# Optimization experiments

Hardware: AMD Instinct MI355X
Metric: run time of the kernel (lower is better)

## Reference

```python
import jax, jax.numpy as jnp
import numpy as np


def setup_inputs() -> dict:
    key = jax.random.key(0)
    k1, k2 = jax.random.split(key)
    B, L, J, N = 8, 32, 128, 512
    ypred = jax.random.normal(k1, (B, L, J, N), dtype=jnp.float32)
    xyz = jax.random.normal(k2, (B, L, N, 3), dtype=jnp.float32)
    return {"ypred": ypred, "xyz": xyz}


def _pairwise_dist(x):
    # x: [BL, N, 3] -> Euclidean distance [BL, N, N] via the mm trick,
    # with the diagonal forced to exactly 0 (matching torch.cdist(x, x)).
    sq = jnp.sum(x * x, axis=-1)                       # [BL, N]
    d2 = sq[:, :, None] + sq[:, None, :] - 2.0 * jnp.einsum('bnd,bmd->bnm', x, x)
    d2 = jnp.maximum(d2, 0.0)
    dist = jnp.sqrt(d2)
    n = x.shape[1]
    eye = jnp.eye(n, dtype=bool)
    return jnp.where(eye[None, :, :], 0.0, dist)


def reference(ypred, xyz):
    B, L, J, N = ypred.shape
    x = xyz.reshape(B * L, N, 3)
    dist = _pairwise_dist(x)                           # [BL, N, N]
    max_idx = jnp.argmax(dist, axis=2)                 # [BL, N] farthest point
    dist_masked = jnp.where(dist == 0.0, 1e6, dist)    # mask self (and exact dupes)
    min_idx = jnp.argmin(dist_masked, axis=2)          # [BL, N] nearest point

    # per-point logit vectors: [BL, N, J]
    yp = jnp.transpose(ypred, (0, 1, 3, 2)).reshape(B * L, N, J)
    sim = jnp.einsum('bnj,bmj->bnm', yp, yp)           # [BL, N, N]

    sim_at_max = jnp.take_along_axis(sim, max_idx[:, :, None], axis=2)[..., 0]
    sim_at_min = jnp.take_along_axis(sim, min_idx[:, :, None], axis=2)[..., 0]
    return jnp.mean(sim_at_max - sim_at_min)
```

## Files before the change

### kernel.cpp

```cpp
#include <hip/hip_runtime.h>

#pragma clang fp contract(off)

#define NBATCH 256
#define NPTS   512
#define JDIM   128
#define NPAIR  (NBATCH * NPTS)
#define NCHUNK 8
#define ROWS   16

__device__ __forceinline__ void gload_lds16(const void* g, void* l) {
    __builtin_amdgcn_global_load_lds(
        (const __attribute__((address_space(1))) void*)g,
        (__attribute__((address_space(3))) void*)l, 16, 0, 0);
}

__global__ __launch_bounds__(512) void fused_kernel(
    const float* __restrict__ ypred,
    const float* __restrict__ xyz,
    float* __restrict__ partials)
{
    __shared__ float4 xyzS[NPTS];
    __shared__ __align__(16) float Lt[3][ROWS * NPTS];
    __shared__ float wredc[NCHUNK][8];

    const int t  = threadIdx.x;
    const int bl = blockIdx.x;
    const float*  xp  = xyz + (size_t)bl * NPTS * 3;
    const float4* src = (const float4*)(ypred + (size_t)bl * JDIM * NPTS);
    const int wbase = t & ~63;

    float ox = xp[3 * t], oy = xp[3 * t + 1], oz = xp[3 * t + 2];
    float oq = (ox * ox + oy * oy) + oz * oz;
    xyzS[t] = make_float4(-2.0f * ox, -2.0f * oy, -2.0f * oz, oq);

    #pragma unroll
    for (int c0 = 0; c0 < 3; ++c0) {
        float4* tile = (float4*)Lt[c0];
        #pragma unroll
        for (int q = 0; q < 4; ++q)
            gload_lds16(src + c0 * 2048 + q * 512 + t, tile + q * 512 + wbase);
    }

    asm volatile("s_waitcnt lgkmcnt(0)" ::: "memory");
    __builtin_amdgcn_s_barrier();

    float bmax = -1.0f, bmin = 3.0e38f;
    int   ima  = 0,     imi  = 0;
    #pragma unroll 8
    for (int m = 0; m < NPTS; ++m) {
        float4 qv = xyzS[m];
        float dt = (ox * qv.x + oy * qv.y) + oz * qv.z;
        float d2 = (oq + qv.w) + dt;
        bool gt = d2 > bmax;
        ima = gt ? m : ima;  bmax = gt ? d2 : bmax;
        bool lt = (d2 < bmin) && (d2 > 0.0f);
        imi = lt ? m : imi;  bmin = lt ? d2 : bmin;
    }
    const int pma = ima, pmi = imi;

    #pragma unroll
    for (int c = 0; c < NCHUNK; ++c) {
        if (c <= 5)      asm volatile("s_waitcnt vmcnt(8)" ::: "memory");
        else if (c == 6) asm volatile("s_waitcnt vmcnt(4)" ::: "memory");
        else             asm volatile("s_waitcnt vmcnt(0)" ::: "memory");
        __builtin_amdgcn_s_barrier();

        const float* L = Lt[c % 3];
        float accP = 0.0f, accM = 0.0f;
        #pragma unroll
        for (int r = 0; r < ROWS; ++r) {
            float a  = L[r * NPTS + t];
            float b  = L[r * NPTS + pma];
            float cm = L[r * NPTS + pmi];
            accP = fmaf(a, b, accP);
            accM = fmaf(a, cm, accM);
        }
        float d = accP - accM;
        #pragma unroll
        for (int off = 32; off > 0; off >>= 1)
            d += __shfl_down(d, off);
        if ((t & 63) == 0) wredc[c][t >> 6] = d;

        if (c + 3 < NCHUNK) {
            __builtin_amdgcn_s_barrier();
            float4* tile = (float4*)Lt[c % 3];
            #pragma unroll
            for (int q = 0; q < 4; ++q)
                gload_lds16(src + (c + 3) * 2048 + q * 512 + t,
                            tile + q * 512 + wbase);
        }
    }

    asm volatile("s_waitcnt lgkmcnt(0)" ::: "memory");
    __builtin_amdgcn_s_barrier();
    if (t < NCHUNK) {
        float ssum = 0.0f;
        #pragma unroll
        for (int w = 0; w < 8; ++w) ssum += wredc[t][w];
        partials[bl * NCHUNK + t] = ssum;
    }
}

__global__ __launch_bounds__(1024) void reduce_mean_kernel(
    const float* __restrict__ partials, float* __restrict__ out)
{
    const int t = threadIdx.x;
    float v = partials[t] + partials[t + 1024];
    #pragma unroll
    for (int off = 32; off > 0; off >>= 1)
        v += __shfl_down(v, off);

    __shared__ float w[16];
    if ((t & 63) == 0) w[t >> 6] = v;
    __syncthreads();
    if (t == 0) {
        float s = 0.0f;
        #pragma unroll
        for (int i = 0; i < 16; ++i) s += w[i];
        out[0] = s * (1.0f / (float)NPAIR);
    }
}

extern "C" void kernel_launch(void* const* d_in, const int* in_sizes, int n_in,
                              void* d_out, int out_size, void* d_ws, size_t ws_size,
                              hipStream_t stream) {
    const float* ypred = (const float*)d_in[0];
    const float* xyz   = (const float*)d_in[1];

    float* partials = (float*)d_ws;
    float* out      = (float*)d_out;

    fused_kernel<<<NBATCH, 512, 0, stream>>>(ypred, xyz, partials);
    reduce_mean_kernel<<<1, 1024, 0, stream>>>(partials, out);
}
```

Measured before the change: 129.1 us.

## Split each batch across two blocks and parallelize argmax/argmin search

Launches two blocks per batch element. Each block handles half of the query points, and its 512 threads split the candidate scan into two halves that are merged through shared memory. The ypred pipeline drops from triple to double buffering with a prefetch one chunk ahead, and partial sums go to a larger buffer that the reduce kernel now sums. The goal is more blocks and less serial scan per thread on a 256-CU GPU. The cost is that every block loads the full ypred tile for its batch, which doubles global traffic, and only half the threads do the dot-product phase.

Measured after the change: 121.2 us. -6.1%, faster.

```diff
diff --git a/kernel.cpp b/kernel.cpp
--- a/kernel.cpp
+++ b/kernel.cpp
@@ -18,37 +18,44 @@
 __global__ __launch_bounds__(512) void fused_kernel(
     const float* __restrict__ ypred,
     const float* __restrict__ xyz,
-    float* __restrict__ partials)
+    float* __restrict__ partials2)
 {
     __shared__ float4 xyzS[NPTS];
-    __shared__ __align__(16) float Lt[3][ROWS * NPTS];
-    __shared__ float wredc[NCHUNK][8];
+    __shared__ __align__(16) float Lt[2][ROWS * NPTS];
+    __shared__ float mxv[256]; __shared__ int mxi[256];
+    __shared__ float mnv[256]; __shared__ int mni[256];
 
     const int t  = threadIdx.x;
-    const int bl = blockIdx.x;
+    const int bl = blockIdx.x & 255;
+    const int h  = blockIdx.x >> 8;
     const float*  xp  = xyz + (size_t)bl * NPTS * 3;
     const float4* src = (const float4*)(ypred + (size_t)bl * JDIM * NPTS);
     const int wbase = t & ~63;
 
-    float ox = xp[3 * t], oy = xp[3 * t + 1], oz = xp[3 * t + 2];
+    {
+        float x = xp[3 * t], y = xp[3 * t + 1], z = xp[3 * t + 2];
+        float sq = (x * x + y * y) + z * z;
+        xyzS[t] = make_float4(-2.0f * x, -2.0f * y, -2.0f * z, sq);
+    }
+
+    const int p  = h * 256 + (t & 255);
+    const int mh = t >> 8;
+    float ox = xp[3 * p], oy = xp[3 * p + 1], oz = xp[3 * p + 2];
     float oq = (ox * ox + oy * oy) + oz * oz;
-    xyzS[t] = make_float4(-2.0f * ox, -2.0f * oy, -2.0f * oz, oq);
 
     #pragma unroll
-    for (int c0 = 0; c0 < 3; ++c0) {
-        float4* tile = (float4*)Lt[c0];
-        #pragma unroll
-        for (int q = 0; q < 4; ++q)
-            gload_lds16(src + c0 * 2048 + q * 512 + t, tile + q * 512 + wbase);
-    }
+    for (int q = 0; q < 4; ++q)
+        gload_lds16(src + q * 512 + t, (float4*)Lt[0] + q * 512 + wbase);
 
     asm volatile("s_waitcnt lgkmcnt(0)" ::: "memory");
     __builtin_amdgcn_s_barrier();
 
+    const int m0 = mh << 8;
     float bmax = -1.0f, bmin = 3.0e38f;
-    int   ima  = 0,     imi  = 0;
+    int   ima  = m0,    imi  = m0;
     #pragma unroll 8
-    for (int m = 0; m < NPTS; ++m) {
+    for (int mm = 0; mm < 256; ++mm) {
+        int m = m0 + mm;
         float4 qv = xyzS[m];
         float dt = (ox * qv.x + oy * qv.y) + oz * qv.z;
         float d2 = (oq + qv.w) + dt;
@@ -57,56 +64,64 @@
         bool lt = (d2 < bmin) && (d2 > 0.0f);
         imi = lt ? m : imi;  bmin = lt ? d2 : bmin;
     }
-    const int pma = ima, pmi = imi;
 
-    #pragma unroll
+    if (t >= 256) {
+        mxv[t - 256] = bmax;  mxi[t - 256] = ima;
+        mnv[t - 256] = bmin;  mni[t - 256] = imi;
+    }
+    __syncthreads();
+    int pma = ima, pmi = imi;
+    if (t < 256) {
+        float v1 = mxv[t];  if (v1 > bmax) pma = mxi[t];
+        float u1 = mnv[t];  if (u1 < bmin) pmi = mni[t];
+    }
+
     for (int c = 0; c < NCHUNK; ++c) {
-        if (c <= 5)      asm volatile("s_waitcnt vmcnt(8)" ::: "memory");
-        else if (c == 6) asm volatile("s_waitcnt vmcnt(4)" ::: "memory");
-        else             asm volatile("s_waitcnt vmcnt(0)" ::: "memory");
+        asm volatile("s_waitcnt vmcnt(0)" ::: "memory");
         __builtin_amdgcn_s_barrier();
 
-        const float* L = Lt[c % 3];
-        float accP = 0.0f, accM = 0.0f;
-        #pragma unroll
-        for (int r = 0; r < ROWS; ++r) {
-            float a  = L[r * NPTS + t];
-            float b  = L[r * NPTS + pma];
-            float cm = L[r * NPTS + pmi];
-            accP = fmaf(a, b, accP);
-            accM = fmaf(a, cm, accM);
-        }
-        float d = accP - accM;
-        #pragma unroll
-        for (int off = 32; off > 0; off >>= 1)
-            d += __shfl_down(d, off);
-        if ((t & 63) == 0) wredc[c][t >> 6] = d;
-
-        if (c + 3 < NCHUNK) {
-            __builtin_amdgcn_s_barrier();
-            float4* tile = (float4*)Lt[c % 3];
+        if (c + 1 < NCHUNK) {
+            float4* tile = (float4*)Lt[(c + 1) & 1];
             #pragma unroll
             for (int q = 0; q < 4; ++q)
-                gload_lds16(src + (c + 3) * 2048 + q * 512 + t,
+                gload_lds16(src + (c + 1) * 2048 + q * 512 + t,
                             tile + q * 512 + wbase);
         }
-    }
 
-    asm volatile("s_waitcnt lgkmcnt(0)" ::: "memory");
-    __builtin_amdgcn_s_barrier();
-    if (t < NCHUNK) {
-        float ssum = 0.0f;
-        #pragma unroll
-        for (int w = 0; w < 8; ++w) ssum += wredc[t][w];
-        partials[bl * NCHUNK + t] = ssum;
+        if (t < 256) {
+            const float* L = Lt[c & 1];
+            const int col = h * 256 + t;
+            float accP = 0.0f, accM = 0.0f;
+            #pragma unroll
+            for (int r = 0; r < ROWS; ++r) {
+                float a  = L[r * NPTS + col];
+                float b  = L[r * NPTS + pma];
+                float cm = L[r * NPTS + pmi];
+                accP = fmaf(a, b, accP);
+                accM = fmaf(a, cm, accM);
+            }
+            float d = accP - accM;
+            #pragma unroll
+            for (int off = 32; off > 0; off >>= 1)
+                d += __shfl_down(d, off);
+            if ((t & 63) == 0)
+                partials2[(size_t)(bl * NCHUNK + c) * 8 + h * 4 + (t >> 6)] = d;
+        }
     }
 }
 
 __global__ __launch_bounds__(1024) void reduce_mean_kernel(
-    const float* __restrict__ partials, float* __restrict__ out)
+    const float* __restrict__ partials2, float* __restrict__ out)
 {
     const int t = threadIdx.x;
-    float v = partials[t] + partials[t + 1024];
+    const float4* p4 = (const float4*)partials2;
+
+    float4 a0 = p4[2 * t],          a1 = p4[2 * t + 1];
+    float4 b0 = p4[2 * (t + 1024)], b1 = p4[2 * (t + 1024) + 1];
+    float fa = ((((((a0.x + a0.y) + a0.z) + a0.w) + a1.x) + a1.y) + a1.z) + a1.w;
+    float fb = ((((((b0.x + b0.y) + b0.z) + b0.w) + b1.x) + b1.y) + b1.z) + b1.w;
+    float v = fa + fb;
+
     #pragma unroll
     for (int off = 32; off > 0; off >>= 1)
         v += __shfl_down(v, off);
@@ -128,9 +143,9 @@
     const float* ypred = (const float*)d_in[0];
     const float* xyz   = (const float*)d_in[1];
 
-    float* partials = (float*)d_ws;
-    float* out      = (float*)d_out;
+    float* partials2 = (float*)d_ws;
+    float* out       = (float*)d_out;
 
-    fused_kernel<<<NBATCH, 512, 0, stream>>>(ypred, xyz, partials);
-    reduce_mean_kernel<<<1, 1024, 0, stream>>>(partials, out);
+    fused_kernel<<<2 * NBATCH, 512, 0, stream>>>(ypred, xyz, partials2);
+    reduce_mean_kernel<<<1, 1024, 0, stream>>>(partials2, out);
 }
```
